# Performance work log

Measured on AMD Instinct MI355X. Metric: run time of the kernel, lower is better.

## Reference

```python
import jax, jax.numpy as jnp
import numpy as np

N_FEAT = 7
N_CLASSES = 2
HIDDEN = 128
N_NODES = 40000
N_EDGES = 640000
N_GRAPHS = 64


def setup_inputs() -> dict:
    key = jax.random.key(0)
    ks = jax.random.split(key, 12)
    x = jax.random.normal(ks[0], (N_NODES, N_FEAT), dtype=jnp.float32)
    edge_index = jax.random.randint(ks[1], (2, N_EDGES), 0, N_NODES, dtype=jnp.int64)
    batch = jnp.sort(jax.random.randint(ks[2], (N_NODES,), 0, N_GRAPHS, dtype=jnp.int64))
    def glorot(k, shape):
        lim = float(np.sqrt(6.0 / (shape[0] + shape[1])))
        return jax.random.uniform(k, shape, jnp.float32, -lim, lim)
    return {
        "x": x, "edge_index": edge_index, "batch": batch,
        "W1": glorot(ks[3], (N_FEAT, HIDDEN)),  "b1": jnp.zeros((HIDDEN,), jnp.float32),
        "W2": glorot(ks[4], (HIDDEN, HIDDEN)),  "b2": jnp.zeros((HIDDEN,), jnp.float32),
        "W3": glorot(ks[5], (HIDDEN, HIDDEN)),  "b3": jnp.zeros((HIDDEN,), jnp.float32),
        "Wl": glorot(ks[6], (HIDDEN, N_CLASSES)), "bl": jnp.zeros((N_CLASSES,), jnp.float32),
    }


def _gcn_norm(edge_index, n_nodes):
    # add self-loops, then symmetric normalization deg^{-1/2} A_hat deg^{-1/2}
    loop = jnp.arange(n_nodes, dtype=edge_index.dtype)
    src = jnp.concatenate([edge_index[0], loop])
    dst = jnp.concatenate([edge_index[1], loop])
    deg = jax.ops.segment_sum(jnp.ones_like(dst, dtype=jnp.float32), dst, num_segments=n_nodes)
    dinv = jax.lax.rsqrt(jnp.maximum(deg, 1.0))
    norm = dinv[src] * dinv[dst]  # [E + N]
    return src, dst, norm


def _gcn_conv(x, W, b, src, dst, norm, n_nodes):
    h = x @ W                                  # [N, out] (transform before propagate)
    msg = h[src] * norm[:, None]               # gather + normalize per edge
    out = jax.ops.segment_sum(msg, dst, num_segments=n_nodes)  # scatter-add
    return out + b


def reference(x, edge_index, batch, W1, b1, W2, b2, W3, b3, Wl, bl):
    n = x.shape[0]
    src, dst, norm = _gcn_norm(edge_index, n)
    h = jax.nn.relu(_gcn_conv(x, W1, b1, src, dst, norm, n))
    h = jax.nn.relu(_gcn_conv(h, W2, b2, src, dst, norm, n))
    h = _gcn_conv(h, W3, b3, src, dst, norm, n)
    # global mean pool over graphs
    sums = jax.ops.segment_sum(h, batch, num_segments=N_GRAPHS)
    cnts = jax.ops.segment_sum(jnp.ones((n,), jnp.float32), batch, num_segments=N_GRAPHS)
    pooled = sums / jnp.maximum(cnts, 1.0)[:, None]
    # dropout is identity in eval mode (training=False)
    return pooled @ Wl + bl
```

## Files before the change

kernel.cpp:

```cpp
#include <hip/hip_runtime.h>
#include <hip/hip_bf16.h>
#include <hip/hip_fp16.h>

#define N_FEAT 7
#define HIDDEN 128
#define N_CLASSES 2
#define N_GRAPHS 64
#define SCAN_TILE 1024

typedef _Float16 half8 __attribute__((ext_vector_type(8)));
typedef float f32x4 __attribute__((ext_vector_type(4)));

__device__ __forceinline__ float4 ldh4(const __half* p) {
    uint2 v = *(const uint2*)p;
    __half2 a = *reinterpret_cast<__half2*>(&v.x);
    __half2 b = *reinterpret_cast<__half2*>(&v.y);
    float2 fa = __half22float2(a), fb = __half22float2(b);
    return make_float4(fa.x, fa.y, fb.x, fb.y);
}
__device__ __forceinline__ void sth4(__half* p, float a, float b, float c, float d) {
    __half2 lo = __floats2half2_rn(a, b);
    __half2 hi = __floats2half2_rn(c, d);
    uint2 v;
    v.x = *reinterpret_cast<unsigned int*>(&lo);
    v.y = *reinterpret_cast<unsigned int*>(&hi);
    *(uint2*)p = v;
}

__global__ void k_zero(int* __restrict__ deg, float* __restrict__ gsum, int n) {
    int i = blockIdx.x * blockDim.x + threadIdx.x;
    if (i < n) deg[i] = 0;
    if (i < N_GRAPHS * HIDDEN) gsum[i] = 0.f;
}

__global__ void k_count(const int* __restrict__ dst, int* __restrict__ deg, int E) {
    int e4 = (blockIdx.x * blockDim.x + threadIdx.x) << 2;
    if (e4 + 4 <= E) {
        int4 d = *(const int4*)&dst[e4];
        atomicAdd(&deg[d.x], 1);
        atomicAdd(&deg[d.y], 1);
        atomicAdd(&deg[d.z], 1);
        atomicAdd(&deg[d.w], 1);
    } else {
        for (int e = e4; e < E; ++e) atomicAdd(&deg[dst[e]], 1);
    }
}

__global__ __launch_bounds__(1024) void k_scan_a(const int* __restrict__ deg,
                                                 int* __restrict__ bsum, int n) {
    __shared__ int s[SCAN_TILE];
    int tid = threadIdx.x;
    int i = blockIdx.x * SCAN_TILE + tid;
    s[tid] = (i < n) ? deg[i] : 0;
    __syncthreads();
#pragma unroll
    for (int off = 512; off > 0; off >>= 1) {
        if (tid < off) s[tid] += s[tid + off];
        __syncthreads();
    }
    if (tid == 0) bsum[blockIdx.x] = s[0];
}

__global__ __launch_bounds__(1024) void k_scan_b(const int* __restrict__ bsum,
                                                 int* __restrict__ boff,
                                                 int* __restrict__ start,
                                                 const int* __restrict__ batch,
                                                 int* __restrict__ goff, int B, int n) {
    __shared__ int s[SCAN_TILE];
    int tid = threadIdx.x;
    int v = (tid < B) ? bsum[tid] : 0;
    s[tid] = v;
    __syncthreads();
    for (int off = 1; off < SCAN_TILE; off <<= 1) {
        int t = (tid >= off) ? s[tid - off] : 0;
        __syncthreads();
        s[tid] += t;
        __syncthreads();
    }
    if (tid < B) boff[tid] = s[tid] - v;
    if (tid == B - 1) start[n] = s[tid];
    if (tid <= N_GRAPHS) {
        int lo = 0, hi = n;
        while (lo < hi) {
            int m = (lo + hi) >> 1;
            if (batch[m] < tid) lo = m + 1; else hi = m;
        }
        goff[tid] = lo;
    }
}

__global__ __launch_bounds__(1024) void k_scan_c(const int* __restrict__ deg,
                                                 const int* __restrict__ boff,
                                                 int* __restrict__ start,
                                                 int* __restrict__ cursor,
                                                 float* __restrict__ dinv,
                                                 const float* __restrict__ x,
                                                 float* __restrict__ xp, int n) {
    __shared__ int s[SCAN_TILE];
    int tid = threadIdx.x;
    int i = blockIdx.x * SCAN_TILE + tid;
    int v = (i < n) ? deg[i] : 0;
    s[tid] = v;
    __syncthreads();
    for (int off = 1; off < SCAN_TILE; off <<= 1) {
        int t = (tid >= off) ? s[tid - off] : 0;
        __syncthreads();
        s[tid] += t;
        __syncthreads();
    }
    if (i < n) {
        int ex = boff[blockIdx.x] + s[tid] - v;
        start[i] = ex;
        cursor[i] = ex;
        float di = rsqrtf((float)(v + 1));
        dinv[i] = di;
#pragma unroll
        for (int j = 0; j < 8; ++j)
            xp[(size_t)i * 8 + j] = (j < N_FEAT) ? di * x[i * N_FEAT + j] : 0.f;
    }
}

__global__ void k_fill(const int* __restrict__ src, const int* __restrict__ dst,
                       int* __restrict__ cursor, int* __restrict__ csr_src, int E) {
    int e4 = (blockIdx.x * blockDim.x + threadIdx.x) << 2;
    if (e4 + 4 <= E) {
        int4 s = *(const int4*)&src[e4];
        int4 d = *(const int4*)&dst[e4];
        csr_src[atomicAdd(&cursor[d.x], 1)] = s.x;
        csr_src[atomicAdd(&cursor[d.y], 1)] = s.y;
        csr_src[atomicAdd(&cursor[d.z], 1)] = s.z;
        csr_src[atomicAdd(&cursor[d.w], 1)] = s.w;
    } else {
        for (int e = e4; e < E; ++e)
            csr_src[atomicAdd(&cursor[dst[e]], 1)] = src[e];
    }
}

__global__ void k_wpack(const float* __restrict__ W2, const float* __restrict__ W3,
                        __half* __restrict__ Whp2, __half* __restrict__ Whp3) {
    int idx = blockIdx.x * blockDim.x + threadIdx.x;
    int sel = idx >> 14;
    int e = idx & 16383;
    int j = e & 7, l = (e >> 3) & 63, kk = (e >> 9) & 3, c = e >> 11;
    int k = kk * 32 + (l >> 4) * 8 + j;
    int col = c * 16 + (l & 15);
    const float* W = sel ? W3 : W2;
    __half* O = sel ? Whp3 : Whp2;
    O[e] = __float2half(W[k * 128 + col]);
}

__global__ __launch_bounds__(256) void k_agg7(const float* __restrict__ xp,
                                              float* __restrict__ ax,
                                              const int* __restrict__ start,
                                              const int* __restrict__ csr_src,
                                              const float* __restrict__ dinv, int nnodes) {
    int t = blockIdx.x * blockDim.x + threadIdx.x;
    int g = t >> 3, j = t & 7;
    if (g >= nnodes) return;
    float acc = xp[(size_t)g * 8 + j];
    int e0 = start[g], e1 = start[g + 1];
    int e = e0;
    for (; e + 4 <= e1; e += 4) {
        int s0 = csr_src[e + 0], s1 = csr_src[e + 1];
        int s2 = csr_src[e + 2], s3 = csr_src[e + 3];
        acc += xp[(size_t)s0 * 8 + j] + xp[(size_t)s1 * 8 + j]
             + xp[(size_t)s2 * 8 + j] + xp[(size_t)s3 * 8 + j];
    }
    for (; e < e1; ++e) acc += xp[(size_t)csr_src[e] * 8 + j];
    ax[(size_t)g * 8 + j] = dinv[g] * acc;
}

__global__ __launch_bounds__(256) void k_gemm7(const float* __restrict__ AX,
                                               const float* __restrict__ W1,
                                               const float* __restrict__ b1,
                                               __half* __restrict__ h1, int n) {
    __shared__ float w[N_FEAT * HIDDEN];
    __shared__ float bs[HIDDEN];
    int tid = threadIdx.x;
    for (int i = tid; i < N_FEAT * HIDDEN; i += 256) w[i] = W1[i];
    if (tid < HIDDEN) bs[tid] = b1[tid];
    __syncthreads();
    int row = blockIdx.x * 2 + (tid >> 7);
    int col = tid & 127;
    if (row >= n) return;
    float acc = bs[col];
#pragma unroll
    for (int k = 0; k < N_FEAT; ++k)
        acc += AX[(size_t)row * 8 + k] * w[k * HIDDEN + col];
    h1[(size_t)row * HIDDEN + col] = __float2half(fmaxf(acc, 0.f));
}

__global__ __launch_bounds__(256) void k_gemm128m(const __half* __restrict__ A16,
                                                  const __half* __restrict__ Whp,
                                                  const float* __restrict__ dinv,
                                                  __half* __restrict__ Ts, int nrows) {
    __shared__ __half ctile[64][128];
    int tid = threadIdx.x;
    int w = tid >> 6;
    int lane = tid & 63;
    int row0 = blockIdx.x * 64;
    int m = lane & 15;
    int kg = lane >> 4;
    f32x4 acc[8];
#pragma unroll
    for (int c = 0; c < 8; ++c) acc[c] = (f32x4){0.f, 0.f, 0.f, 0.f};
    int arow = row0 + w * 16 + m;
#pragma unroll
    for (int kk = 0; kk < 4; ++kk) {
        uint4 av = make_uint4(0u, 0u, 0u, 0u);
        if (arow < nrows)
            av = *(const uint4*)&A16[(size_t)arow * 128 + kk * 32 + kg * 8];
        half8 a = *reinterpret_cast<half8*>(&av);
#pragma unroll
        for (int c = 0; c < 8; ++c) {
            uint4 bv = *(const uint4*)&Whp[((c * 4 + kk) << 9) + lane * 8];
            half8 b = *reinterpret_cast<half8*>(&bv);
            acc[c] = __builtin_amdgcn_mfma_f32_16x16x32_f16(a, b, acc[c], 0, 0, 0);
        }
    }
    int crow = w * 16 + kg * 4;
#pragma unroll
    for (int reg = 0; reg < 4; ++reg) {
        int rr = row0 + crow + reg;
        float sc = (rr < nrows) ? dinv[rr] : 0.f;
#pragma unroll
        for (int c = 0; c < 8; ++c)
            ctile[crow + reg][c * 16 + m] = __float2half(sc * acc[c][reg]);
    }
    __syncthreads();
    const uint4* srcp = (const uint4*)&ctile[0][0];
    uint4* dstp = (uint4*)&Ts[(size_t)row0 * 128];
#pragma unroll
    for (int r = 0; r < 4; ++r) {
        int idx = r * 256 + tid;
        if (row0 + (idx >> 4) < nrows) dstp[idx] = srcp[idx];
    }
}

template<int OUT16>
__global__ __launch_bounds__(256) void k_agg(const __half* __restrict__ Ts,
                                             float* __restrict__ H32,
                                             __half* __restrict__ H16o,
                                             const int* __restrict__ start,
                                             const int* __restrict__ csr_src,
                                             const float* __restrict__ dinv,
                                             const float* __restrict__ bias,
                                             int relu, int nnodes) {
    int g = (blockIdx.x * blockDim.x + threadIdx.x) >> 5;
    int lane = threadIdx.x & 31;
    if (g >= nnodes) return;
    const int loff = lane * 4;
    float4 v = ldh4(&Ts[(size_t)g * 128 + loff]);
    float ax = v.x, ay = v.y, az = v.z, aw = v.w;
    int e0 = start[g], e1 = start[g + 1];
    int e = e0;
    for (; e + 8 <= e1; e += 8) {
        int s[8];
        float4 u[8];
#pragma unroll
        for (int j = 0; j < 8; ++j) s[j] = csr_src[e + j];
#pragma unroll
        for (int j = 0; j < 8; ++j) u[j] = ldh4(&Ts[(size_t)s[j] * 128 + loff]);
#pragma unroll
        for (int j = 0; j < 8; ++j) {
            ax += u[j].x; ay += u[j].y; az += u[j].z; aw += u[j].w;
        }
    }
    if (e + 4 <= e1) {
        int s[4];
        float4 u[4];
#pragma unroll
        for (int j = 0; j < 4; ++j) s[j] = csr_src[e + j];
#pragma unroll
        for (int j = 0; j < 4; ++j) u[j] = ldh4(&Ts[(size_t)s[j] * 128 + loff]);
#pragma unroll
        for (int j = 0; j < 4; ++j) {
            ax += u[j].x; ay += u[j].y; az += u[j].z; aw += u[j].w;
        }
        e += 4;
    }
    for (; e < e1; ++e) {
        float4 u = ldh4(&Ts[(size_t)csr_src[e] * 128 + loff]);
        ax += u.x; ay += u.y; az += u.z; aw += u.w;
    }
    float di = dinv[g];
    float4 b = *(const float4*)&bias[loff];
    ax = di * ax + b.x; ay = di * ay + b.y;
    az = di * az + b.z; aw = di * aw + b.w;
    if (relu) {
        ax = fmaxf(ax, 0.f); ay = fmaxf(ay, 0.f);
        az = fmaxf(az, 0.f); aw = fmaxf(aw, 0.f);
    }
    if (OUT16) {
        sth4(&H16o[(size_t)g * 128 + loff], ax, ay, az, aw);
    } else {
        *(float4*)&H32[(size_t)g * 128 + loff] = make_float4(ax, ay, az, aw);
    }
}

__global__ __launch_bounds__(256) void k_pool2(const float* __restrict__ H,
                                               const int* __restrict__ goff,
                                               float* __restrict__ gsum) {
    int g   = blockIdx.x >> 3;
    int sub = blockIdx.x & 7;
    int grp = threadIdx.x >> 5;
    int lane = threadIdx.x & 31;
    int n0 = goff[g], n1 = goff[g + 1];
    float4 acc = make_float4(0.f, 0.f, 0.f, 0.f);
    for (int n = n0 + sub * 8 + grp; n < n1; n += 64) {
        float4 v = *(const float4*)&H[(size_t)n * 128 + lane * 4];
        acc.x += v.x; acc.y += v.y; acc.z += v.z; acc.w += v.w;
    }
    __shared__ float red[8][128];
    *(float4*)&red[grp][lane * 4] = acc;
    __syncthreads();
    if (grp == 0) {
        float4 t = *(const float4*)&red[0][lane * 4];
#pragma unroll
        for (int k = 1; k < 8; ++k) {
            float4 r = *(const float4*)&red[k][lane * 4];
            t.x += r.x; t.y += r.y; t.z += r.z; t.w += r.w;
        }
        atomicAdd(&gsum[g * HIDDEN + lane * 4 + 0], t.x);
        atomicAdd(&gsum[g * HIDDEN + lane * 4 + 1], t.y);
        atomicAdd(&gsum[g * HIDDEN + lane * 4 + 2], t.z);
        atomicAdd(&gsum[g * HIDDEN + lane * 4 + 3], t.w);
    }
}

__global__ __launch_bounds__(128) void k_final(const float* __restrict__ gsum,
                                               const int* __restrict__ goff,
                                               const float* __restrict__ Wl,
                                               const float* __restrict__ bl,
                                               float* __restrict__ out) {
    int tid = threadIdx.x;
    int g = tid >> 1;
    int c = tid & 1;
    int cnt = goff[g + 1] - goff[g];
    float inv = 1.0f / (float)max(cnt, 1);
    float acc = 0.f;
#pragma unroll 8
    for (int k = 0; k < HIDDEN; ++k)
        acc += gsum[g * HIDDEN + k] * Wl[k * N_CLASSES + c];
    out[g * N_CLASSES + c] = acc * inv + bl[c];
}

extern "C" void kernel_launch(void* const* d_in, const int* in_sizes, int n_in,
                              void* d_out, int out_size, void* d_ws, size_t ws_size,
                              hipStream_t stream) {
    const float* x    = (const float*)d_in[0];
    const int*   ei   = (const int*)d_in[1];
    const int*   batch= (const int*)d_in[2];
    const float* W1   = (const float*)d_in[3];
    const float* b1   = (const float*)d_in[4];
    const float* W2   = (const float*)d_in[5];
    const float* b2   = (const float*)d_in[6];
    const float* W3   = (const float*)d_in[7];
    const float* b3   = (const float*)d_in[8];
    const float* Wl   = (const float*)d_in[9];
    const float* bl   = (const float*)d_in[10];
    float* out = (float*)d_out;

    const int N = in_sizes[0] / N_FEAT;
    const int E = in_sizes[1] / 2;
    const int* e_src = ei;
    const int* e_dst = ei + E;
    const int B = (N + SCAN_TILE - 1) / SCAN_TILE;

    char* ws = (char*)d_ws;
    auto carve = [&](size_t bytes) -> char* {
        char* p = ws;
        ws += (bytes + 255) & ~(size_t)255;
        return p;
    };
    __half* T       = (__half*)carve((size_t)N * HIDDEN * 2);
    __half* H16     = (__half*)carve((size_t)N * HIDDEN * 2);
    float*  H32     = (float*) carve((size_t)N * HIDDEN * 4);
    float*  xp      = (float*) carve((size_t)N * 8 * 4);
    float*  ax      = (float*) carve((size_t)N * 8 * 4);
    int*    deg     = (int*)   carve((size_t)N * 4);
    int*    start   = (int*)   carve((size_t)(N + 1) * 4);
    int*    cursor  = (int*)   carve((size_t)N * 4);
    float*  dinv    = (float*) carve((size_t)N * 4);
    int*    csr_src = (int*)   carve((size_t)E * 4);
    float*  gsum    = (float*) carve((size_t)N_GRAPHS * HIDDEN * 4);
    int*    goff    = (int*)   carve((size_t)(N_GRAPHS + 1) * 4);
    int*    bsum    = (int*)   carve((size_t)B * 4);
    int*    boff    = (int*)   carve((size_t)B * 4);
    __half* Whp2    = (__half*)carve((size_t)HIDDEN * HIDDEN * 2);
    __half* Whp3    = (__half*)carve((size_t)HIDDEN * HIDDEN * 2);
    if ((size_t)(ws - (char*)d_ws) > ws_size) return;

    k_zero  <<<(N + 255) / 256, 256, 0, stream>>>(deg, gsum, N);
    k_count <<<(E / 4 + 255) / 256, 256, 0, stream>>>(e_dst, deg, E);
    k_wpack <<<(2 * HIDDEN * HIDDEN + 255) / 256, 256, 0, stream>>>(W2, W3, Whp2, Whp3);
    k_scan_a<<<B, 1024, 0, stream>>>(deg, bsum, N);
    k_scan_b<<<1, 1024, 0, stream>>>(bsum, boff, start, batch, goff, B, N);
    k_scan_c<<<B, 1024, 0, stream>>>(deg, boff, start, cursor, dinv, x, xp, N);
    k_fill  <<<(E / 4 + 255) / 256, 256, 0, stream>>>(e_src, e_dst, cursor, csr_src, E);

    const int aggBlocks  = (N * 32 + 255) / 256;
    const int gemmBlocks = (N + 63) / 64;

    k_agg7 <<<(N * 8 + 255) / 256, 256, 0, stream>>>(xp, ax, start, csr_src, dinv, N);
    k_gemm7<<<(N + 1) / 2, 256, 0, stream>>>(ax, W1, b1, H16, N);
    k_gemm128m<<<gemmBlocks, 256, 0, stream>>>(H16, Whp2, dinv, T, N);
    k_agg<1>  <<<aggBlocks, 256, 0, stream>>>(T, nullptr, H16, start, csr_src, dinv, b2, 1, N);
    k_gemm128m<<<gemmBlocks, 256, 0, stream>>>(H16, Whp3, dinv, T, N);
    k_agg<0>  <<<aggBlocks, 256, 0, stream>>>(T, H32, nullptr, start, csr_src, dinv, b3, 0, N);
    k_pool2<<<N_GRAPHS * 8, 256, 0, stream>>>(H32, goff, gsum);
    k_final<<<1, 128, 0, stream>>>(gsum, goff, Wl, bl, out);
}
```

Before: 195.6 us.

## Split aggregation into 8 feature slices per node chunk for cache locality

The 128-wide aggregation kernel now assigns each block 64 nodes and one 16-column feature slice, with 4 threads per node instead of 32. Consecutive blocks cover different slices of the same node chunk, so the gathered working set per slice is smaller and should stay resident in L2/MALL. The cost is narrower memory transactions (32 bytes per neighbour row segment), 8x more index loads, and more divergence from degree imbalance within a wave of 16 nodes.

After: 242.6 us. +24.0%, slower.

```diff
diff --git a/kernel.cpp b/kernel.cpp
--- a/kernel.cpp
+++ b/kernel.cpp
@@ -238,19 +238,22 @@
 }
 
 template<int OUT16>
-__global__ __launch_bounds__(256) void k_agg(const __half* __restrict__ Ts,
-                                             float* __restrict__ H32,
-                                             __half* __restrict__ H16o,
-                                             const int* __restrict__ start,
-                                             const int* __restrict__ csr_src,
-                                             const float* __restrict__ dinv,
-                                             const float* __restrict__ bias,
-                                             int relu, int nnodes) {
-    int g = (blockIdx.x * blockDim.x + threadIdx.x) >> 5;
-    int lane = threadIdx.x & 31;
+__global__ __launch_bounds__(256) void k_aggs(const __half* __restrict__ Ts,
+                                              float* __restrict__ H32,
+                                              __half* __restrict__ H16o,
+                                              const int* __restrict__ start,
+                                              const int* __restrict__ csr_src,
+                                              const float* __restrict__ dinv,
+                                              const float* __restrict__ bias,
+                                              int relu, int nnodes) {
+    int slice = blockIdx.x & 7;
+    int chunk = blockIdx.x >> 3;
+    int nl = threadIdx.x >> 2;
+    int l4 = threadIdx.x & 3;
+    int g = chunk * 64 + nl;
     if (g >= nnodes) return;
-    const int loff = lane * 4;
-    float4 v = ldh4(&Ts[(size_t)g * 128 + loff]);
+    const int doff = slice * 16 + l4 * 4;
+    float4 v = ldh4(&Ts[(size_t)g * 128 + doff]);
     float ax = v.x, ay = v.y, az = v.z, aw = v.w;
     int e0 = start[g], e1 = start[g + 1];
     int e = e0;
@@ -260,7 +263,7 @@
 #pragma unroll
         for (int j = 0; j < 8; ++j) s[j] = csr_src[e + j];
 #pragma unroll
-        for (int j = 0; j < 8; ++j) u[j] = ldh4(&Ts[(size_t)s[j] * 128 + loff]);
+        for (int j = 0; j < 8; ++j) u[j] = ldh4(&Ts[(size_t)s[j] * 128 + doff]);
 #pragma unroll
         for (int j = 0; j < 8; ++j) {
             ax += u[j].x; ay += u[j].y; az += u[j].z; aw += u[j].w;
@@ -272,7 +275,7 @@
 #pragma unroll
         for (int j = 0; j < 4; ++j) s[j] = csr_src[e + j];
 #pragma unroll
-        for (int j = 0; j < 4; ++j) u[j] = ldh4(&Ts[(size_t)s[j] * 128 + loff]);
+        for (int j = 0; j < 4; ++j) u[j] = ldh4(&Ts[(size_t)s[j] * 128 + doff]);
 #pragma unroll
         for (int j = 0; j < 4; ++j) {
             ax += u[j].x; ay += u[j].y; az += u[j].z; aw += u[j].w;
@@ -280,11 +283,11 @@
         e += 4;
     }
     for (; e < e1; ++e) {
-        float4 u = ldh4(&Ts[(size_t)csr_src[e] * 128 + loff]);
+        float4 u = ldh4(&Ts[(size_t)csr_src[e] * 128 + doff]);
         ax += u.x; ay += u.y; az += u.z; aw += u.w;
     }
     float di = dinv[g];
-    float4 b = *(const float4*)&bias[loff];
+    float4 b = *(const float4*)&bias[doff];
     ax = di * ax + b.x; ay = di * ay + b.y;
     az = di * az + b.z; aw = di * aw + b.w;
     if (relu) {
@@ -292,9 +295,9 @@
         az = fmaxf(az, 0.f); aw = fmaxf(aw, 0.f);
     }
     if (OUT16) {
-        sth4(&H16o[(size_t)g * 128 + loff], ax, ay, az, aw);
+        sth4(&H16o[(size_t)g * 128 + doff], ax, ay, az, aw);
     } else {
-        *(float4*)&H32[(size_t)g * 128 + loff] = make_float4(ax, ay, az, aw);
+        *(float4*)&H32[(size_t)g * 128 + doff] = make_float4(ax, ay, az, aw);
     }
 }
 
@@ -399,15 +402,15 @@
     k_scan_c<<<B, 1024, 0, stream>>>(deg, boff, start, cursor, dinv, x, xp, N);
     k_fill  <<<(E / 4 + 255) / 256, 256, 0, stream>>>(e_src, e_dst, cursor, csr_src, E);
 
-    const int aggBlocks  = (N * 32 + 255) / 256;
+    const int aggsBlocks = ((N + 63) / 64) * 8;
     const int gemmBlocks = (N + 63) / 64;
 
     k_agg7 <<<(N * 8 + 255) / 256, 256, 0, stream>>>(xp, ax, start, csr_src, dinv, N);
     k_gemm7<<<(N + 1) / 2, 256, 0, stream>>>(ax, W1, b1, H16, N);
     k_gemm128m<<<gemmBlocks, 256, 0, stream>>>(H16, Whp2, dinv, T, N);
-    k_agg<1>  <<<aggBlocks, 256, 0, stream>>>(T, nullptr, H16, start, csr_src, dinv, b2, 1, N);
+    k_aggs<1> <<<aggsBlocks, 256, 0, stream>>>(T, nullptr, H16, start, csr_src, dinv, b2, 1, N);
     k_gemm128m<<<gemmBlocks, 256, 0, stream>>>(H16, Whp3, dinv, T, N);
-    k_agg<0>  <<<aggBlocks, 256, 0, stream>>>(T, H32, nullptr, start, csr_src, dinv, b3, 0, N);
+    k_aggs<0> <<<aggsBlocks, 256, 0, stream>>>(T, H32, nullptr, start, csr_src, dinv, b3, 0, N);
     k_pool2<<<N_GRAPHS * 8, 256, 0, stream>>>(H32, goff, gsum);
     k_final<<<1, 128, 0, stream>>>(gsum, goff, Wl, bl, out);
 }
```
